# Kernel optimization log

Measured on AMD Instinct MI355X. Metric: run time of the kernel, lower is better.

Reference implementation:

```python
import jax, jax.numpy as jnp
import numpy as np

N_TERMS = 10   # hard-coded self.n_terms = 10 in __init__
N_BLOCKS = 4


def conv2d_same(x, k):
    # x: [B,C,H,W], k: [O,I,kh,kw], same padding, stride 1
    ph, pw = (k.shape[2] - 1) // 2, (k.shape[3] - 1) // 2
    return jax.lax.conv_general_dilated(
        x, k, window_strides=(1, 1),
        padding=[(ph, ph), (pw, pw)],
        dimension_numbers=('NCHW', 'OIHW', 'NCHW'))


def conv_exp(x, k, terms=N_TERMS):
    # Truncated power series of the convolution exponential:
    def body(carry, i):
        result, prod = carry
        prod = conv2d_same(prod, k) / i
        return (result + prod, prod), None
    i_vals = jnp.arange(1, terms + 1, dtype=x.dtype)
    (result, _), _ = jax.lax.scan(body, (x, x), i_vals)
    return result


def kernel_log_det(k):
    # log|det| of the conv-exp operator per spatial location:
    # trace of the kernel at its spatial center (convexp log_det)
    mh, mw = (k.shape[2] - 1) // 2, (k.shape[3] - 1) // 2
    return jnp.trace(k[:, :, mh, mw])


def setup_inputs() -> dict:
    key = jax.random.key(0)
    kx, kf = jax.random.split(key)
    B, C, H, W, K = 256, 1, 256, 256, 7
    x = jax.random.normal(kx, (B, C, H, W), dtype=jnp.float32)
    # expanded equivariant filters, one per block; small scale keeps
    # the power series and tanh well-conditioned
    filters = jax.random.normal(kf, (N_BLOCKS, C, C, K, K), dtype=jnp.float32) * 0.05
    return {"x": x, "filters": filters}


def reference(x, filters):
    B, C, H, W = x.shape
    log_det_J = jnp.zeros((B,), dtype=x.dtype)
    z = x
    for i in reversed(range(N_BLOCKS)):
        k = filters[i]
        z = conv_exp(z, k, terms=N_TERMS)
        z = jnp.tanh(z)  # invertible_tanh
        log_det_J = log_det_J - kernel_log_det(k) * (H * W)
    return jnp.squeeze(z), log_det_J.reshape(-1, 1)
```

## Files before the change

### kernel.cpp

```cpp
#include <hip/hip_runtime.h>


typedef _Float16 h2 __attribute__((ext_vector_type(2)));

#define HH 256
#define WW 256
#define NT 10
#define NRINGS 10
#define PITCH 264
#define RING_ELEMS (PITCH * 7)
#define ACCE (NRINGS * RING_ELEMS)
#define ACC_ROWS 42
#define SMEM_U16 (ACCE + ACC_ROWS * WW)
#define FIN_LAG 41
#define T_STEPS 301
#define NTHREADS 704
#define PF 3

union U32H2 { unsigned int u; h2 h; };
static __device__ __forceinline__ h2 uh(unsigned int u) { U32H2 x; x.u = u; return x.h; }
static __device__ __forceinline__ unsigned int hu(h2 h) { U32H2 x; x.h = h; return x.u; }
static __device__ __forceinline__ unsigned int pk2f(float lo, float hi) {
    h2 h; h[0] = (_Float16)lo; h[1] = (_Float16)hi; return hu(h);
}

static __device__ __forceinline__ float dot2f(unsigned int a, unsigned int b, float c) {
#if __has_builtin(__builtin_amdgcn_fdot2)
    return __builtin_amdgcn_fdot2(uh(a), uh(b), c, false);
#else
    h2 ah = uh(a), bh = uh(b);
    return c + (float)ah[0] * (float)bh[0] + (float)ah[1] * (float)bh[1];
#endif
}

static __device__ __forceinline__ float tanh_fast(float x) {
    float e = __expf(2.0f * x);
    return 1.0f - 2.0f / (e + 1.0f);
}

__global__ void prep_kernel(const float* __restrict__ filters,
                            float* __restrict__ logdet,
                            unsigned int* __restrict__ pk) {
    const int tid = threadIdx.x;
    if (tid < 28) {
        const int blk = tid / 7, ky = tid - blk * 7;
        const float* w = filters + blk * 49 + ky * 7;
        unsigned int* o = pk + blk * 64 + ky * 8;
        o[0] = pk2f(0.f, w[0]);  o[1] = pk2f(w[1], w[2]);
        o[2] = pk2f(w[3], w[4]); o[3] = pk2f(w[5], w[6]);
        o[4] = pk2f(w[0], w[1]); o[5] = pk2f(w[2], w[3]);
        o[6] = pk2f(w[4], w[5]); o[7] = pk2f(w[6], 0.f);
    }
    const float c = -(float)(HH * WW) *
        (filters[24] + filters[49 + 24] + filters[98 + 24] + filters[147 + 24]);
    for (int j = tid; j < 256; j += blockDim.x) logdet[j] = c;
}

template <int IN_F16, int OUT_F16>
__global__ __launch_bounds__(NTHREADS)
void cascade_kernel(const void* __restrict__ in_, void* __restrict__ out_,
                    const unsigned int* __restrict__ pkg) {
    __shared__ __align__(16) unsigned short smem[SMEM_U16];
    const int tid = threadIdx.x;
    const int wav = tid >> 6;
    const int lane = tid & 63;
    const int img = blockIdx.x;

    {
        unsigned int* s4 = (unsigned int*)smem;
        for (int i = tid; i < SMEM_U16 / 2; i += NTHREADS) s4[i] = 0u;
    }

    unsigned int Kc[56];
#pragma unroll
    for (int i = 0; i < 56; ++i)
        Kc[i] = __builtin_amdgcn_readfirstlane(pkg[i]);

    const bool is_stage = (wav < NT);
    const bool is_util = (wav == NT);
    const int stg = wav + 1;
    const float sinv = 1.0f / (float)stg;
    const int rb_in = wav * RING_ELEMS;
    const int rb_out = (wav + 1) * RING_ELEMS;

    int rdIdx[7], wrIdx[7];
#pragma unroll
    for (int u = 0; u < 7; ++u) {
        const int sR = (((u + 3 - 4 * stg) % 7) + 7) % 7;
        const int sW = (((u - 4 * stg) % 7) + 7) % 7;
        rdIdx[u] = rb_in + sR * PITCH + 4 * lane;
        wrIdx[u] = rb_out + sW * PITCH + 4 + 4 * lane;
    }

    unsigned int win[7][6];
#pragma unroll
    for (int a = 0; a < 7; ++a)
#pragma unroll
        for (int b = 0; b < 6; ++b) win[a][b] = 0u;

    const int ACC_END = ACCE + ACC_ROWS * WW;
    int accS = ACCE + ((((-4 * stg) % ACC_ROWS) + ACC_ROWS) % ACC_ROWS) * WW + 4 * lane;
    int accI = ACCE + 4 * lane;
    int accF = ACCE + 1 * WW + 4 * lane;

    const unsigned short* gin16 = (const unsigned short*)in_ + (size_t)img * (HH * WW);
    const float* gin32 = (const float*)in_ + (size_t)img * (HH * WW);
    unsigned short* gout16 = (unsigned short*)out_ + (size_t)img * (HH * WW);
    float* gout32 = (float*)out_ + (size_t)img * (HH * WW);

    uint2 zh[7]; float4 zf[7];
    if (is_util) {
#pragma unroll
        for (int r = 0; r < PF; ++r) {
            if (IN_F16) zh[r] = *(const uint2*)(gin16 + r * WW + 4 * lane);
            else        zf[r] = *(const float4*)(gin32 + r * WW + 4 * lane);
        }
    }
    __syncthreads();

    for (int t0 = 0; t0 < T_STEPS; t0 += 7) {
#pragma unroll
        for (int u = 0; u < 7; ++u) {
            const int t = t0 + u;
            if (is_stage) {
                const int q = t - 4 * stg;
                {
                    const uint2* p = (const uint2*)&smem[rdIdx[u]];
                    const uint2 A = p[0], B = p[1], C = p[2];
                    win[(u + 6) % 7][0] = A.x; win[(u + 6) % 7][1] = A.y;
                    win[(u + 6) % 7][2] = B.x; win[(u + 6) % 7][3] = B.y;
                    win[(u + 6) % 7][4] = C.x; win[(u + 6) % 7][5] = C.y;
                }
                if (q >= 0 && q < HH) {
                    float o0 = 0.f, o1 = 0.f, o2 = 0.f, o3 = 0.f;
#pragma unroll
                    for (int ky = 0; ky < 7; ++ky) {
                        const unsigned int v0 = win[(u + ky) % 7][0], v1 = win[(u + ky) % 7][1],
                                           v2 = win[(u + ky) % 7][2], v3 = win[(u + ky) % 7][3],
                                           v4 = win[(u + ky) % 7][4], v5 = win[(u + ky) % 7][5];
                        const unsigned int P0 = Kc[ky * 8 + 0], P1 = Kc[ky * 8 + 1],
                                           P2 = Kc[ky * 8 + 2], P3 = Kc[ky * 8 + 3],
                                           P4 = Kc[ky * 8 + 4], P5 = Kc[ky * 8 + 5],
                                           P6 = Kc[ky * 8 + 6], P7 = Kc[ky * 8 + 7];
                        o0 = dot2f(v0, P0, o0); o0 = dot2f(v1, P1, o0);
                        o0 = dot2f(v2, P2, o0); o0 = dot2f(v3, P3, o0);
                        o1 = dot2f(v1, P4, o1); o1 = dot2f(v2, P5, o1);
                        o1 = dot2f(v3, P6, o1); o1 = dot2f(v4, P7, o1);
                        o2 = dot2f(v1, P0, o2); o2 = dot2f(v2, P1, o2);
                        o2 = dot2f(v3, P2, o2); o2 = dot2f(v4, P3, o2);
                        o3 = dot2f(v2, P4, o3); o3 = dot2f(v3, P5, o3);
                        o3 = dot2f(v4, P6, o3); o3 = dot2f(v5, P7, o3);
                    }
                    o0 *= sinv; o1 *= sinv; o2 *= sinv; o3 *= sinv;
                    uint2 w; w.x = pk2f(o0, o1); w.y = pk2f(o2, o3);
                    if (stg < NT) *(uint2*)&smem[wrIdx[u]] = w;
                    const uint2 av = *(const uint2*)&smem[accS];
                    const h2 lo = uh(av.x) + uh(w.x), hi = uh(av.y) + uh(w.y);
                    uint2 nv; nv.x = hu(lo); nv.y = hu(hi);
                    *(uint2*)&smem[accS] = nv;
                } else if (q >= HH && q <= HH + 2 && stg < NT) {
                    uint2 w; w.x = 0u; w.y = 0u;
                    *(uint2*)&smem[wrIdx[u]] = w;
                }
                accS += WW; if (accS >= ACC_END) accS -= ACC_ROWS * WW;
            } else if (is_util) {
                if (t + PF < HH) {
                    if (IN_F16) zh[(u + PF) % 7] = *(const uint2*)(gin16 + (size_t)(t + PF) * WW + 4 * lane);
                    else        zf[(u + PF) % 7] = *(const float4*)(gin32 + (size_t)(t + PF) * WW + 4 * lane);
                }
                if (t <= HH + 2) {
                    uint2 w;
                    if (t < HH) {
                        if (IN_F16) w = zh[u];
                        else { const float4 g = zf[u]; w.x = pk2f(g.x, g.y); w.y = pk2f(g.z, g.w); }
                    } else { w.x = 0u; w.y = 0u; }
                    *(uint2*)&smem[u * PITCH + 4 + 4 * lane] = w;
                    if (t < HH) *(uint2*)&smem[accI] = w;
                }
                const int f = t - FIN_LAG;
                if (f >= 0 && f < HH) {
                    const uint2 av = *(const uint2*)&smem[accF];
                    const h2 a = uh(av.x), b = uh(av.y);
                    const float r0 = tanh_fast((float)a[0]), r1 = tanh_fast((float)a[1]);
                    const float r2 = tanh_fast((float)b[0]), r3 = tanh_fast((float)b[1]);
                    if (OUT_F16) {
                        uint2 w; w.x = pk2f(r0, r1); w.y = pk2f(r2, r3);
                        *(uint2*)(gout16 + (size_t)f * WW + 4 * lane) = w;
                    } else {
                        float4 w; w.x = r0; w.y = r1; w.z = r2; w.w = r3;
                        *(float4*)(gout32 + (size_t)f * WW + 4 * lane) = w;
                    }
                }
                accI += WW; if (accI >= ACC_END) accI -= ACC_ROWS * WW;
                accF += WW; if (accF >= ACC_END) accF -= ACC_ROWS * WW;
            }
            __syncthreads();
        }
    }
}

extern "C" void kernel_launch(void* const* d_in, const int* in_sizes, int n_in,
                              void* d_out, int out_size, void* d_ws, size_t ws_size,
                              hipStream_t stream) {
    (void)in_sizes; (void)n_in; (void)out_size; (void)ws_size;
    const float* x = (const float*)d_in[0];
    const float* fl = (const float*)d_in[1];
    float* out = (float*)d_out;
    float* logdet = out + (size_t)256 * 256 * 256;

    unsigned short* bufA = (unsigned short*)d_ws;
    unsigned short* bufB = (unsigned short*)d_out;
    unsigned int* pk = (unsigned int*)((char*)d_ws + (size_t)256 * 256 * 256 * 2);

    prep_kernel<<<1, 64, 0, stream>>>(fl, logdet, pk);
    cascade_kernel<0, 1><<<256, NTHREADS, 0, stream>>>(x,    bufA, pk + 3 * 64);
    cascade_kernel<1, 1><<<256, NTHREADS, 0, stream>>>(bufA, bufB, pk + 2 * 64);
    cascade_kernel<1, 1><<<256, NTHREADS, 0, stream>>>(bufB, bufA, pk + 1 * 64);
    cascade_kernel<1, 0><<<256, NTHREADS, 0, stream>>>(bufA, out,  pk + 0 * 64);
}
```

Baseline: 968.6 us.

## Compute 7x7 conv rows with MFMA 16x16x32 f16 using Toeplitz B fragments

Replaces the per-lane fdot2 convolution with MFMA 16x16x32 f16 instructions. Filter taps are pre-expanded into banded Toeplitz fragments, with the 1/stage scale folded in. The ring layout changes so each lane loads 8 contiguous halves, and the pitch is widened. Output is now scattered as scalar f16 stores and read-modify-write accumulations instead of packed uint2, which adds LDS traffic and possible bank conflicts. Scaling the weights in f16 also changes rounding.

Measured after the change: 996.8 us. 2.9% more time.

```diff
diff --git a/kernel.cpp b/kernel.cpp
--- a/kernel.cpp
+++ b/kernel.cpp
@@ -2,12 +2,14 @@
 
 
 typedef _Float16 h2 __attribute__((ext_vector_type(2)));
+typedef _Float16 f16x8 __attribute__((ext_vector_type(8)));
+typedef float f32x4 __attribute__((ext_vector_type(4)));
 
 #define HH 256
 #define WW 256
 #define NT 10
 #define NRINGS 10
-#define PITCH 264
+#define PITCH 272
 #define RING_ELEMS (PITCH * 7)
 #define ACCE (NRINGS * RING_ELEMS)
 #define ACC_ROWS 42
@@ -18,21 +20,15 @@
 #define PF 3
 
 union U32H2 { unsigned int u; h2 h; };
+union U4F8 { uint4 u; f16x8 h; };
+union USH { unsigned short u; _Float16 h; };
+
 static __device__ __forceinline__ h2 uh(unsigned int u) { U32H2 x; x.u = u; return x.h; }
 static __device__ __forceinline__ unsigned int hu(h2 h) { U32H2 x; x.h = h; return x.u; }
 static __device__ __forceinline__ unsigned int pk2f(float lo, float hi) {
     h2 h; h[0] = (_Float16)lo; h[1] = (_Float16)hi; return hu(h);
 }
 
-static __device__ __forceinline__ float dot2f(unsigned int a, unsigned int b, float c) {
-#if __has_builtin(__builtin_amdgcn_fdot2)
-    return __builtin_amdgcn_fdot2(uh(a), uh(b), c, false);
-#else
-    h2 ah = uh(a), bh = uh(b);
-    return c + (float)ah[0] * (float)bh[0] + (float)ah[1] * (float)bh[1];
-#endif
-}
-
 static __device__ __forceinline__ float tanh_fast(float x) {
     float e = __expf(2.0f * x);
     return 1.0f - 2.0f / (e + 1.0f);
@@ -40,16 +36,19 @@
 
 __global__ void prep_kernel(const float* __restrict__ filters,
                             float* __restrict__ logdet,
-                            unsigned int* __restrict__ pk) {
+                            unsigned short* __restrict__ pkB) {
     const int tid = threadIdx.x;
-    if (tid < 28) {
-        const int blk = tid / 7, ky = tid - blk * 7;
+    for (int i = tid; i < 4 * 7 * 64; i += 256) {
+        const int blk = i / 448, r = i - blk * 448, ky = r >> 6, lane = r & 63;
         const float* w = filters + blk * 49 + ky * 7;
-        unsigned int* o = pk + blk * 64 + ky * 8;
-        o[0] = pk2f(0.f, w[0]);  o[1] = pk2f(w[1], w[2]);
-        o[2] = pk2f(w[3], w[4]); o[3] = pk2f(w[5], w[6]);
-        o[4] = pk2f(w[0], w[1]); o[5] = pk2f(w[2], w[3]);
-        o[6] = pk2f(w[4], w[5]); o[7] = pk2f(w[6], 0.f);
+        const int g = lane >> 4, n = lane & 15;
+        unsigned short* o = pkB + (size_t)i * 8;
+        for (int e = 0; e < 8; ++e) {
+            const int tap = 8 * g + e - n - 5;
+            const float v = (tap >= 0 && tap < 7) ? w[tap] : 0.f;
+            USH c; c.h = (_Float16)v;
+            o[e] = c.u;
+        }
     }
     const float c = -(float)(HH * WW) *
         (filters[24] + filters[49 + 24] + filters[98 + 24] + filters[147 + 24]);
@@ -59,47 +58,56 @@
 template <int IN_F16, int OUT_F16>
 __global__ __launch_bounds__(NTHREADS)
 void cascade_kernel(const void* __restrict__ in_, void* __restrict__ out_,
-                    const unsigned int* __restrict__ pkg) {
+                    const uint4* __restrict__ pkBg) {
     __shared__ __align__(16) unsigned short smem[SMEM_U16];
     const int tid = threadIdx.x;
     const int wav = tid >> 6;
     const int lane = tid & 63;
     const int img = blockIdx.x;
+    const int g = lane >> 4, n = lane & 15;
 
     {
         unsigned int* s4 = (unsigned int*)smem;
         for (int i = tid; i < SMEM_U16 / 2; i += NTHREADS) s4[i] = 0u;
     }
 
-    unsigned int Kc[56];
-#pragma unroll
-    for (int i = 0; i < 56; ++i)
-        Kc[i] = __builtin_amdgcn_readfirstlane(pkg[i]);
-
     const bool is_stage = (wav < NT);
     const bool is_util = (wav == NT);
     const int stg = wav + 1;
-    const float sinv = 1.0f / (float)stg;
     const int rb_in = wav * RING_ELEMS;
     const int rb_out = (wav + 1) * RING_ELEMS;
+
+    f16x8 B[7];
+    if (is_stage) {
+        const _Float16 sh = (_Float16)(1.0f / (float)stg);
+        f16x8 sv;
+#pragma unroll
+        for (int j = 0; j < 8; ++j) sv[j] = sh;
+#pragma unroll
+        for (int ky = 0; ky < 7; ++ky) {
+            U4F8 raw; raw.u = pkBg[ky * 64 + lane];
+            B[ky] = raw.h * sv;
+        }
+    }
 
     int rdIdx[7], wrIdx[7];
 #pragma unroll
     for (int u = 0; u < 7; ++u) {
         const int sR = (((u + 3 - 4 * stg) % 7) + 7) % 7;
         const int sW = (((u - 4 * stg) % 7) + 7) % 7;
-        rdIdx[u] = rb_in + sR * PITCH + 4 * lane;
-        wrIdx[u] = rb_out + sW * PITCH + 4 + 4 * lane;
-    }
-
-    unsigned int win[7][6];
+        rdIdx[u] = rb_in + sR * PITCH + 16 * n + 8 * g;
+        wrIdx[u] = rb_out + sW * PITCH + 8 + 64 * g + n;
+    }
+    const int accCol = 64 * g + n;
+
+    f16x8 win[7];
 #pragma unroll
     for (int a = 0; a < 7; ++a)
 #pragma unroll
-        for (int b = 0; b < 6; ++b) win[a][b] = 0u;
+        for (int b = 0; b < 8; ++b) win[a][b] = (_Float16)0.f;
 
     const int ACC_END = ACCE + ACC_ROWS * WW;
-    int accS = ACCE + ((((-4 * stg) % ACC_ROWS) + ACC_ROWS) % ACC_ROWS) * WW + 4 * lane;
+    int accS = ACCE + ((((-4 * stg) % ACC_ROWS) + ACC_ROWS) % ACC_ROWS) * WW + accCol;
     int accI = ACCE + 4 * lane;
     int accF = ACCE + 1 * WW + 4 * lane;
 
@@ -124,43 +132,24 @@
             const int t = t0 + u;
             if (is_stage) {
                 const int q = t - 4 * stg;
-                {
-                    const uint2* p = (const uint2*)&smem[rdIdx[u]];
-                    const uint2 A = p[0], B = p[1], C = p[2];
-                    win[(u + 6) % 7][0] = A.x; win[(u + 6) % 7][1] = A.y;
-                    win[(u + 6) % 7][2] = B.x; win[(u + 6) % 7][3] = B.y;
-                    win[(u + 6) % 7][4] = C.x; win[(u + 6) % 7][5] = C.y;
-                }
+                win[(u + 6) % 7] = *(const f16x8*)&smem[rdIdx[u]];
                 if (q >= 0 && q < HH) {
-                    float o0 = 0.f, o1 = 0.f, o2 = 0.f, o3 = 0.f;
-#pragma unroll
-                    for (int ky = 0; ky < 7; ++ky) {
-                        const unsigned int v0 = win[(u + ky) % 7][0], v1 = win[(u + ky) % 7][1],
-                                           v2 = win[(u + ky) % 7][2], v3 = win[(u + ky) % 7][3],
-                                           v4 = win[(u + ky) % 7][4], v5 = win[(u + ky) % 7][5];
-                        const unsigned int P0 = Kc[ky * 8 + 0], P1 = Kc[ky * 8 + 1],
-                                           P2 = Kc[ky * 8 + 2], P3 = Kc[ky * 8 + 3],
-                                           P4 = Kc[ky * 8 + 4], P5 = Kc[ky * 8 + 5],
-                                           P6 = Kc[ky * 8 + 6], P7 = Kc[ky * 8 + 7];
-                        o0 = dot2f(v0, P0, o0); o0 = dot2f(v1, P1, o0);
-                        o0 = dot2f(v2, P2, o0); o0 = dot2f(v3, P3, o0);
-                        o1 = dot2f(v1, P4, o1); o1 = dot2f(v2, P5, o1);
-                        o1 = dot2f(v3, P6, o1); o1 = dot2f(v4, P7, o1);
-                        o2 = dot2f(v1, P0, o2); o2 = dot2f(v2, P1, o2);
-                        o2 = dot2f(v3, P2, o2); o2 = dot2f(v4, P3, o2);
-                        o3 = dot2f(v2, P4, o3); o3 = dot2f(v3, P5, o3);
-                        o3 = dot2f(v4, P6, o3); o3 = dot2f(v5, P7, o3);
+                    f32x4 D = {0.f, 0.f, 0.f, 0.f};
+#pragma unroll
+                    for (int ky = 0; ky < 7; ++ky)
+                        D = __builtin_amdgcn_mfma_f32_16x16x32_f16(
+                                win[(u + ky) % 7], B[ky], D, 0, 0, 0);
+#pragma unroll
+                    for (int r = 0; r < 3 + 1; ++r) {
+                        const _Float16 hv = (_Float16)D[r];
+                        if (stg < NT) *(_Float16*)&smem[wrIdx[u] + 16 * r] = hv;
+                        _Float16* ap = (_Float16*)&smem[accS + 16 * r];
+                        *ap = *ap + hv;
                     }
-                    o0 *= sinv; o1 *= sinv; o2 *= sinv; o3 *= sinv;
-                    uint2 w; w.x = pk2f(o0, o1); w.y = pk2f(o2, o3);
-                    if (stg < NT) *(uint2*)&smem[wrIdx[u]] = w;
-                    const uint2 av = *(const uint2*)&smem[accS];
-                    const h2 lo = uh(av.x) + uh(w.x), hi = uh(av.y) + uh(w.y);
-                    uint2 nv; nv.x = hu(lo); nv.y = hu(hi);
-                    *(uint2*)&smem[accS] = nv;
                 } else if (q >= HH && q <= HH + 2 && stg < NT) {
-                    uint2 w; w.x = 0u; w.y = 0u;
-                    *(uint2*)&smem[wrIdx[u]] = w;
+#pragma unroll
+                    for (int r = 0; r < 4; ++r)
+                        *(_Float16*)&smem[wrIdx[u] + 16 * r] = (_Float16)0.f;
                 }
                 accS += WW; if (accS >= ACC_END) accS -= ACC_ROWS * WW;
             } else if (is_util) {
@@ -172,9 +161,9 @@
                     uint2 w;
                     if (t < HH) {
                         if (IN_F16) w = zh[u];
-                        else { const float4 g = zf[u]; w.x = pk2f(g.x, g.y); w.y = pk2f(g.z, g.w); }
+                        else { const float4 gz = zf[u]; w.x = pk2f(gz.x, gz.y); w.y = pk2f(gz.z, gz.w); }
                     } else { w.x = 0u; w.y = 0u; }
-                    *(uint2*)&smem[u * PITCH + 4 + 4 * lane] = w;
+                    *(uint2*)&smem[u * PITCH + 8 + 4 * lane] = w;
                     if (t < HH) *(uint2*)&smem[accI] = w;
                 }
                 const int f = t - FIN_LAG;
@@ -210,11 +199,12 @@
 
     unsigned short* bufA = (unsigned short*)d_ws;
     unsigned short* bufB = (unsigned short*)d_out;
-    unsigned int* pk = (unsigned int*)((char*)d_ws + (size_t)256 * 256 * 256 * 2);
-
-    prep_kernel<<<1, 64, 0, stream>>>(fl, logdet, pk);
-    cascade_kernel<0, 1><<<256, NTHREADS, 0, stream>>>(x,    bufA, pk + 3 * 64);
-    cascade_kernel<1, 1><<<256, NTHREADS, 0, stream>>>(bufA, bufB, pk + 2 * 64);
-    cascade_kernel<1, 1><<<256, NTHREADS, 0, stream>>>(bufB, bufA, pk + 1 * 64);
-    cascade_kernel<1, 0><<<256, NTHREADS, 0, stream>>>(bufA, out,  pk + 0 * 64);
-}
+    unsigned short* pkB = (unsigned short*)((char*)d_ws + (size_t)256 * 256 * 256 * 2);
+
+    prep_kernel<<<1, 256, 0, stream>>>(fl, logdet, pkB);
+    const uint4* pb = (const uint4*)pkB;
+    cascade_kernel<0, 1><<<256, NTHREADS, 0, stream>>>(x,    bufA, pb + 3 * 448);
+    cascade_kernel<1, 1><<<256, NTHREADS, 0, stream>>>(bufA, bufB, pb + 2 * 448);
+    cascade_kernel<1, 1><<<256, NTHREADS, 0, stream>>>(bufB, bufA, pb + 1 * 448);
+    cascade_kernel<1, 0><<<256, NTHREADS, 0, stream>>>(bufA, out,  pb + 0 * 448);
+}
```
